# Optimization experiments

Measured on AMD Instinct MI355X. Metric: run time of the kernel, lower is better.

## Reference

```python
import jax, jax.numpy as jnp
import numpy as np

B, S, H, DH = 8, 1024, 16, 64
D = H * DH  # d_model = 1024
M_ALPHA = -1e9


def setup_inputs() -> dict:
    key = jax.random.key(0)
    ks = jax.random.split(key, 11)
    scale = 1.0 / np.sqrt(D)
    x = jax.random.normal(ks[0], (B, S, D), dtype=jnp.float32)
    # 0/1 padding mask, shape [B, S, 1] (1 = masked position)
    mask = (jax.random.uniform(ks[1], (B, S, 1)) < 0.25).astype(jnp.float32)
    mk = lambda k: jax.random.normal(k, (D, D), dtype=jnp.float32) * scale
    return {
        "x": x,
        "mask": mask,
        "wq_w": mk(ks[2]), "wq_b": jnp.zeros((D,), jnp.float32),
        "wk_w": mk(ks[3]), "wk_b": jnp.zeros((D,), jnp.float32),
        "wv_w": mk(ks[4]), "wv_b": jnp.zeros((D,), jnp.float32),
        "wo_w": mk(ks[5]), "wo_b": jnp.zeros((D,), jnp.float32),
    }


def _split_heads(t):
    # [B, S, D] -> [B, H, S, DH]
    return t.reshape(B, S, H, DH).transpose(0, 2, 1, 3)


def reference(x, mask, wq_w, wq_b, wk_w, wk_b, wv_w, wv_b, wo_w, wo_b):
    q = _split_heads(x @ wq_w + wq_b)  # [B,H,S,DH]
    k = _split_heads(x @ wk_w + wk_b)
    v = _split_heads(x @ wv_w + wv_b)

    logits = jnp.einsum("bhqd,bhkd->bhqk", q, k) / jnp.sqrt(
        jnp.asarray(DH, jnp.float32))
    qk_values = logits  # pre-mask scaled logits (temperature == 0.0 -> no-op)

    # QK mask path: mask [B,S,1] -> tile to [B,S,S] rows (m[b,i,j] = mask[b,i]),
    # then symmetrize (square) -> mask[b,i] + mask[b,j], clamp at 1.
    m = mask[:, :, 0]                               # [B,S]
    mask_qk = jnp.minimum(1.0, m[:, :, None] + m[:, None, :])  # [B,S,S]
    logits = logits + mask_qk[:, None, :, :] * M_ALPHA

    attn = jax.nn.softmax(logits, axis=-1)          # [B,H,S,S]
    z = jnp.einsum("bhqk,bhkd->bhqd", attn, v)      # [B,H,S,DH]
    z = z.transpose(0, 2, 1, 3).reshape(B, S, D)
    out = z @ wo_w + wo_b
    return (out, attn, qk_values, q, k, v)
```

## Files before the change

### kernel.cpp

```cpp
#include <hip/hip_runtime.h>
#include <hip/hip_bf16.h>
#include <stdint.h>

#define BB 8
#define SS 1024
#define HH 16
#define DHD 64
#define DD 1024

typedef __attribute__((ext_vector_type(8))) short bf16x8;
typedef __attribute__((ext_vector_type(4))) float f32x4;

__device__ __forceinline__ unsigned short f2bf(float f) {
  unsigned u = __builtin_bit_cast(unsigned, f);
  u += 0x7fffu + ((u >> 16) & 1u);
  return (unsigned short)(u >> 16);
}

__device__ __forceinline__ unsigned swz(unsigned a) { return a ^ ((a >> 3) & 0x70u); }

#define GLOAD16(gp, lp)                                                        \
  __builtin_amdgcn_global_load_lds(                                            \
      (const __attribute__((address_space(1))) unsigned int*)(gp),             \
      (__attribute__((address_space(3))) unsigned int*)(lp), 16, 0, 0)

#define MFMA16(a, b, c) __builtin_amdgcn_mfma_f32_16x16x32_bf16(a, b, c, 0, 0, 0)

__global__ __launch_bounds__(256) void cvt_x_kernel(const float* __restrict__ x,
                                                    unsigned short* __restrict__ xb) {
  int i = blockIdx.x * 256 + threadIdx.x;
  float4 v = ((const float4*)x)[i];
  ushort4 o;
  o.x = f2bf(v.x); o.y = f2bf(v.y); o.z = f2bf(v.z); o.w = f2bf(v.w);
  ((ushort4*)xb)[i] = o;
}

__global__ __launch_bounds__(256) void transpose_w_kernel(
    const float* __restrict__ w0, const float* __restrict__ w1,
    const float* __restrict__ w2, const float* __restrict__ w3,
    unsigned short* __restrict__ o0, unsigned short* __restrict__ o1,
    unsigned short* __restrict__ o2, unsigned short* __restrict__ o3) {
  __shared__ float tile[32][33];
  const float* src; unsigned short* dst;
  if (blockIdx.z == 0)      { src = w0; dst = o0; }
  else if (blockIdx.z == 1) { src = w1; dst = o1; }
  else if (blockIdx.z == 2) { src = w2; dst = o2; }
  else                      { src = w3; dst = o3; }
  int n0 = blockIdx.x * 32, k0 = blockIdx.y * 32;
  int tx = threadIdx.x, ty = threadIdx.y;
#pragma unroll
  for (int j = 0; j < 32; j += 8)
    tile[ty + j][tx] = src[(size_t)(k0 + ty + j) * DD + n0 + tx];
  __syncthreads();
#pragma unroll
  for (int j = 0; j < 32; j += 8)
    dst[(size_t)(n0 + ty + j) * DD + k0 + tx] = f2bf(tile[tx][ty + j]);
}

__global__ __launch_bounds__(256) void proj_gemm_kernel(
    const unsigned short* __restrict__ xb,
    const unsigned short* __restrict__ wqt, const unsigned short* __restrict__ wkt,
    const unsigned short* __restrict__ wvt,
    const float* __restrict__ bq, const float* __restrict__ bk, const float* __restrict__ bv,
    float* __restrict__ qo, float* __restrict__ ko, float* __restrict__ vo,
    unsigned short* __restrict__ qb, unsigned short* __restrict__ kbf,
    unsigned short* __restrict__ vt) {
  __shared__ __align__(128) unsigned short smem[2 * 128 * 64];
  unsigned short* As = smem;
  unsigned short* Bs = smem + 128 * 64;
  const int tid = threadIdx.x, lane = tid & 63, w = tid >> 6;
  const int wr = (w >> 1) * 64, wc = (w & 1) * 64;
  const int m0 = blockIdx.x * 128;
  const int mat = blockIdx.y >> 3;
  const int n0 = (blockIdx.y & 7) * 128;
  const unsigned short* Bg = (mat == 0) ? wqt : (mat == 1) ? wkt : wvt;
  const float* bias = (mat == 0) ? bq : (mat == 1) ? bk : bv;

  f32x4 acc[4][4];
  f32x4 z4 = {0.f, 0.f, 0.f, 0.f};
#pragma unroll
  for (int i = 0; i < 4; ++i)
#pragma unroll
    for (int j = 0; j < 4; ++j) acc[i][j] = z4;

  for (int kt = 0; kt < 1024; kt += 64) {
    __syncthreads();
#pragma unroll
    for (int i = 0; i < 4; ++i) {
      unsigned obase = (unsigned)(w * 4096 + i * 1024);
      unsigned a = swz(obase + (unsigned)lane * 16);
      GLOAD16((const char*)xb + ((size_t)(m0 + (int)(a >> 7)) * 1024 + kt) * 2 + (a & 127),
              (char*)As + obase);
      GLOAD16((const char*)Bg + ((size_t)(n0 + (int)(a >> 7)) * 1024 + kt) * 2 + (a & 127),
              (char*)Bs + obase);
    }
    __syncthreads();
#pragma unroll
    for (int ks = 0; ks < 2; ++ks) {
      bf16x8 af[4], bfr[4];
#pragma unroll
      for (int mi = 0; mi < 4; ++mi) {
        unsigned a = (unsigned)((wr + mi * 16 + (lane & 15)) * 128 + ks * 64 + ((lane >> 4) * 16));
        af[mi] = *(const bf16x8*)((const char*)As + swz(a));
      }
#pragma unroll
      for (int ni = 0; ni < 4; ++ni) {
        unsigned a = (unsigned)((wc + ni * 16 + (lane & 15)) * 128 + ks * 64 + ((lane >> 4) * 16));
        bfr[ni] = *(const bf16x8*)((const char*)Bs + swz(a));
      }
#pragma unroll
      for (int mi = 0; mi < 4; ++mi)
#pragma unroll
        for (int ni = 0; ni < 4; ++ni)
          acc[mi][ni] = MFMA16(af[mi], bfr[ni], acc[mi][ni]);
    }
  }

  float* fo = (mat == 0) ? qo : (mat == 1) ? ko : vo;
  __syncthreads();
  unsigned short* T = smem;

#pragma unroll
  for (int mi = 0; mi < 4; ++mi)
#pragma unroll
    for (int ni = 0; ni < 4; ++ni) {
      int col = n0 + wc + ni * 16 + (lane & 15);
      float bs = bias[col];
#pragma unroll
      for (int r = 0; r < 4; ++r) {
        int row = m0 + wr + mi * 16 + ((lane >> 4) << 2) + r;
        float v = acc[mi][ni][r] + bs;
        int b = row >> 10, s = row & 1023, h = col >> 6, dh = col & 63;
        size_t bh = (size_t)(b * HH + h);
        __builtin_nontemporal_store(v, &fo[(bh * SS + s) * DHD + dh]);
        if (mat == 2) {
          int sl = wr + mi * 16 + ((lane >> 4) << 2) + r;
          int dl = wc + ni * 16 + (lane & 15);
          T[dl * 128 + (sl ^ ((dl & 7) << 4))] = f2bf(v);
        } else if (mat == 0) {
          qb[(bh * SS + s) * DHD + dh] = f2bf(v * 0.125f);
        } else {
          kbf[(bh * SS + s) * DHD + dh] = f2bf(v);
        }
      }
    }

  if (mat == 2) {
    __syncthreads();
    int row = tid >> 1;
    int half = tid & 1;
    int colg = n0 + row;
    int h2 = colg >> 6, dh2 = colg & 63;
    int b = m0 >> 10;
    int sg0 = (m0 & 1023) + half * 64;
    unsigned short* dst = vt + (((size_t)(b * HH + h2)) * DHD + dh2) * SS + sg0;
#pragma unroll
    for (int j = 0; j < 8; ++j) {
      int sc = half * 64 + j * 8;
      bf16x8 vv = *(const bf16x8*)&T[row * 128 + (sc ^ ((row & 7) << 4))];
      *(bf16x8*)(dst + j * 8) = vv;
    }
  }
}

__global__ __launch_bounds__(256) void attn_kernel(
    const unsigned short* __restrict__ qb, const unsigned short* __restrict__ kb,
    const unsigned short* __restrict__ vt, const float* __restrict__ mask,
    float* __restrict__ qk_out, float* __restrict__ attn_out,
    unsigned short* __restrict__ zb) {
  __shared__ __align__(128) unsigned short kbuf[64 * 64];
  __shared__ __align__(128) unsigned short vbuf[64 * 64];
  __shared__ __align__(128) unsigned short pbuf[4][16 * 64];
  __shared__ __align__(16) float mbuf[SS];

  const int tid = threadIdx.x, lane = tid & 63, w = tid >> 6;
  const int fid = blockIdx.x;
  const int bh = fid & 127, qt = fid >> 7;
  const int b = bh >> 4, h = bh & 15;
  const int r0 = qt * 64 + w * 16;

  ((float4*)mbuf)[tid] = ((const float4*)(mask + (size_t)b * SS))[tid];

  bf16x8 aq[2];
  {
    const unsigned short* p = qb + (size_t)bh * SS * DHD + (size_t)(r0 + (lane & 15)) * DHD + ((lane >> 4) * 8);
    aq[0] = *(const bf16x8*)p;
    aq[1] = *(const bf16x8*)(p + 32);
  }
  float mq[4];
#pragma unroll
  for (int r = 0; r < 4; ++r)
    mq[r] = mask[(size_t)b * SS + r0 + ((lane >> 4) << 2) + r];

  const unsigned short* kbase = kb + (size_t)bh * SS * DHD;
  const char* vbase = (const char*)(vt + (size_t)bh * DHD * SS);
  float* qkb = qk_out + (size_t)bh * SS * SS;
  float* atb = attn_out + (size_t)bh * SS * SS;

  float m_run[4], l_run[4];
#pragma unroll
  for (int r = 0; r < 4; ++r) { m_run[r] = -INFINITY; l_run[r] = 0.f; }

  for (int kt = 0; kt < 16; ++kt) {
    int k0 = kt * 64;
    __syncthreads();
#pragma unroll
    for (int i = 0; i < 2; ++i) {
      unsigned obase = (unsigned)(w * 2048 + i * 1024);
      unsigned a = swz(obase + (unsigned)lane * 16);
      GLOAD16((const char*)(kbase + (size_t)k0 * 64) + a, (char*)kbuf + obase);
    }
    __syncthreads();
    float sm[4][4];
#pragma unroll
    for (int ct = 0; ct < 4; ++ct) {
      f32x4 acc = {0.f, 0.f, 0.f, 0.f};
#pragma unroll
      for (int ks = 0; ks < 2; ++ks) {
        unsigned a = (unsigned)((ct * 16 + (lane & 15)) * 128 + ks * 64 + ((lane >> 4) * 16));
        bf16x8 bk = *(const bf16x8*)((const char*)kbuf + swz(a));
        acc = MFMA16(aq[ks], bk, acc);
      }
      int col = k0 + ct * 16 + (lane & 15);
      float mk = mbuf[col];
      float* qrow = qkb + (size_t)(r0 + ((lane >> 4) << 2)) * SS + col;
#pragma unroll
      for (int r = 0; r < 4; ++r) {
        float logit = acc[r];
        __builtin_nontemporal_store(logit, &qrow[(size_t)r * SS]);
        float t = fminf(mq[r] + mk, 1.f);
        sm[ct][r] = logit + t * (-1.0e9f);
      }
    }
#pragma unroll
    for (int r = 0; r < 4; ++r) {
      float mx = fmaxf(fmaxf(sm[0][r], sm[1][r]), fmaxf(sm[2][r], sm[3][r]));
#pragma unroll
      for (int d = 1; d < 16; d <<= 1) mx = fmaxf(mx, __shfl_xor(mx, d, 64));
      float m_new = fmaxf(m_run[r], mx);
      float es = __expf(sm[0][r] - m_new) + __expf(sm[1][r] - m_new) +
                 __expf(sm[2][r] - m_new) + __expf(sm[3][r] - m_new);
#pragma unroll
      for (int d = 1; d < 16; d <<= 1) es += __shfl_xor(es, d, 64);
      l_run[r] = l_run[r] * __expf(m_run[r] - m_new) + es;
      m_run[r] = m_new;
    }
  }

  float inv_l[4];
#pragma unroll
  for (int r = 0; r < 4; ++r) inv_l[r] = 1.0f / l_run[r];

  f32x4 zacc[4];
#pragma unroll
  for (int dt = 0; dt < 4; ++dt) zacc[dt] = (f32x4){0.f, 0.f, 0.f, 0.f};

  for (int kt = 0; kt < 16; ++kt) {
    int k0 = kt * 64;
    __syncthreads();
#pragma unroll
    for (int i = 0; i < 2; ++i) {
      unsigned obase = (unsigned)(w * 2048 + i * 1024);
      unsigned a = swz(obase + (unsigned)lane * 16);
      GLOAD16((const char*)(kbase + (size_t)k0 * 64) + a, (char*)kbuf + obase);
      GLOAD16(vbase + (size_t)(a >> 7) * (SS * 2) + (size_t)k0 * 2 + (a & 127),
              (char*)vbuf + obase);
    }
    __syncthreads();
#pragma unroll
    for (int ct = 0; ct < 4; ++ct) {
      f32x4 acc = {0.f, 0.f, 0.f, 0.f};
#pragma unroll
      for (int ks = 0; ks < 2; ++ks) {
        unsigned a = (unsigned)((ct * 16 + (lane & 15)) * 128 + ks * 64 + ((lane >> 4) * 16));
        bf16x8 bk = *(const bf16x8*)((const char*)kbuf + swz(a));
        acc = MFMA16(aq[ks], bk, acc);
      }
      int col = k0 + ct * 16 + (lane & 15);
      float mk = mbuf[col];
#pragma unroll
      for (int r = 0; r < 4; ++r) {
        float logit = acc[r];
        float t = fminf(mq[r] + mk, 1.f);
        float e = __expf(logit + t * (-1.0e9f) - m_run[r]);
        float pn = e * inv_l[r];
        __builtin_nontemporal_store(pn, &atb[(size_t)(r0 + ((lane >> 4) << 2) + r) * SS + col]);
        unsigned a2 = (unsigned)((((lane >> 4) << 2) + r) * 128 + (ct * 16 + (lane & 15)) * 2);
        *(unsigned short*)((char*)pbuf[w] + swz(a2)) = f2bf(pn);
      }
    }
#pragma unroll
    for (int dt = 0; dt < 4; ++dt) {
#pragma unroll
      for (int ks = 0; ks < 2; ++ks) {
        unsigned ap = (unsigned)((lane & 15) * 128 + ks * 64 + ((lane >> 4) * 16));
        bf16x8 pa = *(const bf16x8*)((const char*)pbuf[w] + swz(ap));
        unsigned av = (unsigned)((dt * 16 + (lane & 15)) * 128 + ks * 64 + ((lane >> 4) * 16));
        bf16x8 bv = *(const bf16x8*)((const char*)vbuf + swz(av));
        zacc[dt] = MFMA16(pa, bv, zacc[dt]);
      }
    }
  }

#pragma unroll
  for (int dt = 0; dt < 4; ++dt)
#pragma unroll
    for (int r = 0; r < 4; ++r) {
      int srow = r0 + ((lane >> 4) << 2) + r;
      int dcol = dt * 16 + (lane & 15);
      zb[((size_t)b * SS + srow) * DD + h * 64 + dcol] = f2bf(zacc[dt][r]);
    }
}

__global__ __launch_bounds__(256) void out_gemm_kernel(
    const unsigned short* __restrict__ zb, const unsigned short* __restrict__ wot,
    const float* __restrict__ bo, float* __restrict__ outp) {
  __shared__ __align__(128) unsigned short As[128 * 64];
  __shared__ __align__(128) unsigned short Bs[128 * 64];
  const int tid = threadIdx.x, lane = tid & 63, w = tid >> 6;
  const int wr = (w >> 1) * 64, wc = (w & 1) * 64;
  const int m0 = blockIdx.x * 128;
  const int n0 = blockIdx.y * 128;

  f32x4 acc[4][4];
  f32x4 z4 = {0.f, 0.f, 0.f, 0.f};
#pragma unroll
  for (int i = 0; i < 4; ++i)
#pragma unroll
    for (int j = 0; j < 4; ++j) acc[i][j] = z4;

  for (int kt = 0; kt < 1024; kt += 64) {
    __syncthreads();
#pragma unroll
    for (int i = 0; i < 4; ++i) {
      unsigned obase = (unsigned)(w * 4096 + i * 1024);
      unsigned a = swz(obase + (unsigned)lane * 16);
      GLOAD16((const char*)zb + ((size_t)(m0 + (int)(a >> 7)) * 1024 + kt) * 2 + (a & 127),
              (char*)As + obase);
      GLOAD16((const char*)wot + ((size_t)(n0 + (int)(a >> 7)) * 1024 + kt) * 2 + (a & 127),
              (char*)Bs + obase);
    }
    __syncthreads();
#pragma unroll
    for (int ks = 0; ks < 2; ++ks) {
      bf16x8 af[4], bfr[4];
#pragma unroll
      for (int mi = 0; mi < 4; ++mi) {
        unsigned a = (unsigned)((wr + mi * 16 + (lane & 15)) * 128 + ks * 64 + ((lane >> 4) * 16));
        af[mi] = *(const bf16x8*)((const char*)As + swz(a));
      }
#pragma unroll
      for (int ni = 0; ni < 4; ++ni) {
        unsigned a = (unsigned)((wc + ni * 16 + (lane & 15)) * 128 + ks * 64 + ((lane >> 4) * 16));
        bfr[ni] = *(const bf16x8*)((const char*)Bs + swz(a));
      }
#pragma unroll
      for (int mi = 0; mi < 4; ++mi)
#pragma unroll
        for (int ni = 0; ni < 4; ++ni)
          acc[mi][ni] = MFMA16(af[mi], bfr[ni], acc[mi][ni]);
    }
  }
#pragma unroll
  for (int mi = 0; mi < 4; ++mi)
#pragma unroll
    for (int ni = 0; ni < 4; ++ni) {
      int col = n0 + wc + ni * 16 + (lane & 15);
      float bs = bo[col];
#pragma unroll
      for (int r = 0; r < 4; ++r) {
        int row = m0 + wr + mi * 16 + ((lane >> 4) << 2) + r;
        __builtin_nontemporal_store(acc[mi][ni][r] + bs, &outp[(size_t)row * DD + col]);
      }
    }
}

extern "C" void kernel_launch(void* const* d_in, const int* in_sizes, int n_in,
                              void* d_out, int out_size, void* d_ws, size_t ws_size,
                              hipStream_t stream) {
  const float* x    = (const float*)d_in[0];
  const float* mask = (const float*)d_in[1];
  const float* wq_w = (const float*)d_in[2];
  const float* wq_b = (const float*)d_in[3];
  const float* wk_w = (const float*)d_in[4];
  const float* wk_b = (const float*)d_in[5];
  const float* wv_w = (const float*)d_in[6];
  const float* wv_b = (const float*)d_in[7];
  const float* wo_w = (const float*)d_in[8];
  const float* wo_b = (const float*)d_in[9];

  float* outp = (float*)d_out;
  float* attn = outp + (size_t)8388608;
  float* qk   = attn + (size_t)134217728;
  float* qo   = qk + (size_t)134217728;
  float* ko   = qo + (size_t)8388608;
  float* vo   = ko + (size_t)8388608;

  char* ws = (char*)d_ws;
  unsigned short* xb  = (unsigned short*)(ws + 0);
  unsigned short* wqt = (unsigned short*)(ws + 16777216);
  unsigned short* wkt = (unsigned short*)(ws + 18874368);
  unsigned short* wvt = (unsigned short*)(ws + 20971520);
  unsigned short* wot = (unsigned short*)(ws + 23068672);
  unsigned short* qb  = (unsigned short*)(ws + 25165824);
  unsigned short* kb  = (unsigned short*)(ws + 41943040);
  unsigned short* vt  = (unsigned short*)(ws + 58720256);
  unsigned short* zb  = (unsigned short*)(ws + 75497472);

  cvt_x_kernel<<<8192, 256, 0, stream>>>(x, xb);
  transpose_w_kernel<<<dim3(32, 32, 4), dim3(32, 8), 0, stream>>>(
      wq_w, wk_w, wv_w, wo_w, wqt, wkt, wvt, wot);
  proj_gemm_kernel<<<dim3(64, 24), 256, 0, stream>>>(
      xb, wqt, wkt, wvt, wq_b, wk_b, wv_b, qo, ko, vo, qb, kb, vt);
  attn_kernel<<<2048, 256, 0, stream>>>(qb, kb, vt, mask, qk, attn, zb);
  out_gemm_kernel<<<dim3(64, 8), 256, 0, stream>>>(zb, wot, wo_b, outp);
}
```

Measured before the change: 522.3 us.

## Transpose QK MFMA output so each lane owns a row for vectorized stores

Swaps the MFMA operand order in the QK product so each lane holds four consecutive key columns of one query row. The qk and attn fp32 outputs can then be written as 16-byte nontemporal vector stores instead of scalar strided stores. Softmax statistics become a single scalar per lane, reduced across lane groups with two shuffles instead of four. The bf16 P tile is written as packed 8-byte LDS stores with a simpler swizzle. The mask for key columns is now read as a float4 from LDS, which adds a barrier after the mask load.

```diff
diff --git a/kernel.cpp b/kernel.cpp
--- a/kernel.cpp
+++ b/kernel.cpp
@@ -178,28 +178,27 @@
   const int bh = fid & 127, qt = fid >> 7;
   const int b = bh >> 4, h = bh & 15;
   const int r0 = qt * 64 + w * 16;
+  const int q15 = lane & 15, G = lane >> 4;
 
   ((float4*)mbuf)[tid] = ((const float4*)(mask + (size_t)b * SS))[tid];
+  __syncthreads();
 
   bf16x8 aq[2];
   {
-    const unsigned short* p = qb + (size_t)bh * SS * DHD + (size_t)(r0 + (lane & 15)) * DHD + ((lane >> 4) * 8);
+    const unsigned short* p = qb + (size_t)bh * SS * DHD + (size_t)(r0 + q15) * DHD + G * 8;
     aq[0] = *(const bf16x8*)p;
     aq[1] = *(const bf16x8*)(p + 32);
   }
-  float mq[4];
-#pragma unroll
-  for (int r = 0; r < 4; ++r)
-    mq[r] = mask[(size_t)b * SS + r0 + ((lane >> 4) << 2) + r];
+  const float mq = mbuf[r0 + q15];
 
   const unsigned short* kbase = kb + (size_t)bh * SS * DHD;
   const char* vbase = (const char*)(vt + (size_t)bh * DHD * SS);
   float* qkb = qk_out + (size_t)bh * SS * SS;
   float* atb = attn_out + (size_t)bh * SS * SS;
-
-  float m_run[4], l_run[4];
-#pragma unroll
-  for (int r = 0; r < 4; ++r) { m_run[r] = -INFINITY; l_run[r] = 0.f; }
+  float* qrow = qkb + (size_t)(r0 + q15) * SS;
+  float* arow = atb + (size_t)(r0 + q15) * SS;
+
+  float m_run = -INFINITY, l_run = 0.f;
 
   for (int kt = 0; kt < 16; ++kt) {
     int k0 = kt * 64;
@@ -211,49 +210,52 @@
       GLOAD16((const char*)(kbase + (size_t)k0 * 64) + a, (char*)kbuf + obase);
     }
     __syncthreads();
-    float sm[4][4];
+    f32x4 sm[4];
 #pragma unroll
     for (int ct = 0; ct < 4; ++ct) {
       f32x4 acc = {0.f, 0.f, 0.f, 0.f};
 #pragma unroll
       for (int ks = 0; ks < 2; ++ks) {
-        unsigned a = (unsigned)((ct * 16 + (lane & 15)) * 128 + ks * 64 + ((lane >> 4) * 16));
+        unsigned a = (unsigned)((ct * 16 + q15) * 128 + ks * 64 + G * 16);
         bf16x8 bk = *(const bf16x8*)((const char*)kbuf + swz(a));
-        acc = MFMA16(aq[ks], bk, acc);
-      }
-      int col = k0 + ct * 16 + (lane & 15);
-      float mk = mbuf[col];
-      float* qrow = qkb + (size_t)(r0 + ((lane >> 4) << 2)) * SS + col;
+        acc = MFMA16(bk, aq[ks], acc);
+      }
+      int c0 = k0 + ct * 16 + G * 4;
+      __builtin_nontemporal_store(acc, (f32x4*)(qrow + c0));
+      float4 mk4 = *(const float4*)(mbuf + c0);
 #pragma unroll
       for (int r = 0; r < 4; ++r) {
-        float logit = acc[r];
-        __builtin_nontemporal_store(logit, &qrow[(size_t)r * SS]);
-        float t = fminf(mq[r] + mk, 1.f);
-        sm[ct][r] = logit + t * (-1.0e9f);
-      }
-    }
-#pragma unroll
-    for (int r = 0; r < 4; ++r) {
-      float mx = fmaxf(fmaxf(sm[0][r], sm[1][r]), fmaxf(sm[2][r], sm[3][r]));
-#pragma unroll
-      for (int d = 1; d < 16; d <<= 1) mx = fmaxf(mx, __shfl_xor(mx, d, 64));
-      float m_new = fmaxf(m_run[r], mx);
-      float es = __expf(sm[0][r] - m_new) + __expf(sm[1][r] - m_new) +
-                 __expf(sm[2][r] - m_new) + __expf(sm[3][r] - m_new);
-#pragma unroll
-      for (int d = 1; d < 16; d <<= 1) es += __shfl_xor(es, d, 64);
-      l_run[r] = l_run[r] * __expf(m_run[r] - m_new) + es;
-      m_run[r] = m_new;
-    }
-  }
-
-  float inv_l[4];
-#pragma unroll
-  for (int r = 0; r < 4; ++r) inv_l[r] = 1.0f / l_run[r];
+        float t = fminf(mq + ((const float*)&mk4)[r], 1.f);
+        sm[ct][r] = acc[r] + t * (-1.0e9f);
+      }
+    }
+    float mx = sm[0][0];
+#pragma unroll
+    for (int ct = 0; ct < 4; ++ct)
+#pragma unroll
+      for (int r = 0; r < 4; ++r) mx = fmaxf(mx, sm[ct][r]);
+    mx = fmaxf(mx, __shfl_xor(mx, 16, 64));
+    mx = fmaxf(mx, __shfl_xor(mx, 32, 64));
+    float m_new = fmaxf(m_run, mx);
+    float es = 0.f;
+#pragma unroll
+    for (int ct = 0; ct < 4; ++ct)
+#pragma unroll
+      for (int r = 0; r < 4; ++r) es += __expf(sm[ct][r] - m_new);
+    es += __shfl_xor(es, 16, 64);
+    es += __shfl_xor(es, 32, 64);
+    l_run = l_run * __expf(m_run - m_new) + es;
+    m_run = m_new;
+  }
+
+  const float inv_l = 1.0f / l_run;
 
   f32x4 zacc[4];
 #pragma unroll
   for (int dt = 0; dt < 4; ++dt) zacc[dt] = (f32x4){0.f, 0.f, 0.f, 0.f};
+
+  unsigned short* pw = pbuf[w];
+  const unsigned pswz = (unsigned)((q15 & 14) << 3);
 
   for (int kt = 0; kt < 16; ++kt) {
     int k0 = kt * 64;
@@ -272,32 +274,35 @@
       f32x4 acc = {0.f, 0.f, 0.f, 0.f};
 #pragma unroll
       for (int ks = 0; ks < 2; ++ks) {
-        unsigned a = (unsigned)((ct * 16 + (lane & 15)) * 128 + ks * 64 + ((lane >> 4) * 16));
+        unsigned a = (unsigned)((ct * 16 + q15) * 128 + ks * 64 + G * 16);
         bf16x8 bk = *(const bf16x8*)((const char*)kbuf + swz(a));
-        acc = MFMA16(aq[ks], bk, acc);
-      }
-      int col = k0 + ct * 16 + (lane & 15);
-      float mk = mbuf[col];
+        acc = MFMA16(bk, aq[ks], acc);
+      }
+      int c0 = k0 + ct * 16 + G * 4;
+      float4 mk4 = *(const float4*)(mbuf + c0);
+      f32x4 pn;
 #pragma unroll
       for (int r = 0; r < 4; ++r) {
-        float logit = acc[r];
-        float t = fminf(mq[r] + mk, 1.f);
-        float e = __expf(logit + t * (-1.0e9f) - m_run[r]);
-        float pn = e * inv_l[r];
-        __builtin_nontemporal_store(pn, &atb[(size_t)(r0 + ((lane >> 4) << 2) + r) * SS + col]);
-        unsigned a2 = (unsigned)((((lane >> 4) << 2) + r) * 128 + (ct * 16 + (lane & 15)) * 2);
-        *(unsigned short*)((char*)pbuf[w] + swz(a2)) = f2bf(pn);
-      }
-    }
+        float t = fminf(mq + ((const float*)&mk4)[r], 1.f);
+        pn[r] = __expf(acc[r] + t * (-1.0e9f) - m_run) * inv_l;
+      }
+      __builtin_nontemporal_store(pn, (f32x4*)(arow + c0));
+      unsigned u0 = (unsigned)f2bf(pn[0]) | ((unsigned)f2bf(pn[1]) << 16);
+      unsigned u1 = (unsigned)f2bf(pn[2]) | ((unsigned)f2bf(pn[3]) << 16);
+      uint2 pkd = {u0, u1};
+      *(uint2*)((char*)pw + (((unsigned)(q15 * 128 + ct * 32 + G * 8)) ^ pswz)) = pkd;
+    }
+    bf16x8 pa[2];
+#pragma unroll
+    for (int ks = 0; ks < 2; ++ks)
+      pa[ks] = *(const bf16x8*)((char*)pw + (((unsigned)(q15 * 128 + ks * 64 + G * 16)) ^ pswz));
 #pragma unroll
     for (int dt = 0; dt < 4; ++dt) {
 #pragma unroll
       for (int ks = 0; ks < 2; ++ks) {
-        unsigned ap = (unsigned)((lane & 15) * 128 + ks * 64 + ((lane >> 4) * 16));
-        bf16x8 pa = *(const bf16x8*)((const char*)pbuf[w] + swz(ap));
-        unsigned av = (unsigned)((dt * 16 + (lane & 15)) * 128 + ks * 64 + ((lane >> 4) * 16));
+        unsigned av = (unsigned)((dt * 16 + q15) * 128 + ks * 64 + G * 16);
         bf16x8 bv = *(const bf16x8*)((const char*)vbuf + swz(av));
-        zacc[dt] = MFMA16(pa, bv, zacc[dt]);
+        zacc[dt] = MFMA16(pa[ks], bv, zacc[dt]);
       }
     }
   }
@@ -306,8 +311,8 @@
   for (int dt = 0; dt < 4; ++dt)
 #pragma unroll
     for (int r = 0; r < 4; ++r) {
-      int srow = r0 + ((lane >> 4) << 2) + r;
-      int dcol = dt * 16 + (lane & 15);
+      int srow = r0 + G * 4 + r;
+      int dcol = dt * 16 + q15;
       zb[((size_t)b * SS + srow) * DD + h * 64 + dcol] = f2bf(zacc[dt][r]);
     }
 }
```

New measurement: 523.1 us. No clear change (+0.2%).
